# Performance work log

Measured on AMD Instinct MI355X. Metric: run time of the kernel, lower is better.

Reference implementation:

```python
import jax, jax.numpy as jnp
import numpy as np

B, T, DIM, H, L = 16, 4096, 256, 128, 3  # hidden = dim // 2, 3 bidirectional layers


def setup_inputs() -> dict:
    key = jax.random.key(0)
    kx, ki, kh, kb = jax.random.split(key, 4)
    x = jax.random.normal(kx, (B, T, DIM), dtype=jnp.float32)
    # stacked params: [layer, direction(0=fwd,1=bwd), ...]; gates packed as (r, z, n)
    Wi = jax.random.normal(ki, (L, 2, DIM, 3 * H), dtype=jnp.float32) / np.sqrt(DIM).astype(np.float32)
    Wh = jax.random.normal(kh, (L, 2, H, 3 * H), dtype=jnp.float32) / np.sqrt(H).astype(np.float32)
    bh = jax.random.normal(kb, (L, 2, 3 * H), dtype=jnp.float32) * 0.01
    return {"x": x, "Wi": Wi, "Wh": Wh, "bh": bh}


def _gru_dir(x, Wi, Wh, bh, reverse):
    """Run a GRU over time; x [B,T,D] -> h sequence [B,T,H].

    flax nnx.GRUCell math: input denses have no bias, hidden denses have bias;
    n-gate hidden contribution (incl. its bias) is gated by r.
    """
    # precompute all input-side gate projections in one big GEMM (efficient)
    xg = jnp.einsum('btd,dk->btk', x, Wi)  # [B,T,3H]
    Whr, Whz, Whn = jnp.split(Wh, 3, axis=1)
    bhr, bhz, bhn = jnp.split(bh, 3)

    def step(h, xg_t):
        xr, xz, xn = jnp.split(xg_t, 3, axis=-1)
        r = jax.nn.sigmoid(xr + h @ Whr + bhr)
        z = jax.nn.sigmoid(xz + h @ Whz + bhz)
        n = jnp.tanh(xn + r * (h @ Whn + bhn))
        h_new = (1.0 - z) * n + z * h
        return h_new, h_new

    h0 = jnp.zeros((x.shape[0], Whr.shape[0]), x.dtype)
    _, ys = jax.lax.scan(step, h0, jnp.swapaxes(xg, 0, 1), reverse=reverse)
    return jnp.swapaxes(ys, 0, 1)  # [B,T,H], time-aligned with input (keep_order)


def reference(x, Wi, Wh, bh):
    n_layers = Wi.shape[0]
    for l in range(n_layers):
        fwd = _gru_dir(x, Wi[l, 0], Wh[l, 0], bh[l, 0], reverse=False)
        bwd = _gru_dir(x, Wi[l, 1], Wh[l, 1], bh[l, 1], reverse=True)
        x = jnp.concatenate([fwd, bwd], axis=-1)  # [B,T,2H]=[B,T,DIM]
    return x
```

## Files before the change

### kernel.cpp

```cpp
#include <hip/hip_runtime.h>

#define BB 16
#define TT 4096
#define DD 256
#define HH 128
#define G3 384
#define MM (BB*TT)

typedef unsigned short u16;
typedef unsigned int u32;
typedef __attribute__((ext_vector_type(8))) short short8;
typedef __attribute__((ext_vector_type(4))) float f32x4;
typedef __attribute__((ext_vector_type(2))) unsigned int u32x2;

__device__ __forceinline__ float bf2f(u16 u) {
    return __uint_as_float(((u32)u) << 16);
}
__device__ __forceinline__ u16 f2bf(float f) {
    u32 u = __float_as_uint(f);
    u32 lsb = (u >> 16) & 1u;
    u += 0x7fffu + lsb;
    return (u16)(u >> 16);
}

#define Bb 128
#define Bn 128
#define Bk 16

__global__ __launch_bounds__(256) void gemm_in(const float* __restrict__ X,
                                               const float* __restrict__ Wi,
                                               float* __restrict__ XG) {
    __shared__ __align__(16) float As[Bk][Bb + 4];
    __shared__ __align__(16) float Bs[Bk][Bn + 4];
    const int tid = threadIdx.x;
    const int m0  = blockIdx.y * Bb;
    const int nb  = blockIdx.x;
    const int n0  = nb * Bn;
    const int dir = (n0 >= G3) ? 1 : 0;
    const int nloc0 = n0 - dir * G3;
    const float* Wd = Wi + (size_t)dir * DD * G3;

    const int tx = tid & 15;
    const int ty = tid >> 4;
    float acc[8][8];
    #pragma unroll
    for (int i = 0; i < 8; ++i)
        #pragma unroll
        for (int j = 0; j < 8; ++j) acc[i][j] = 0.f;

    for (int k0 = 0; k0 < DD; k0 += Bk) {
        #pragma unroll
        for (int p = 0; p < 2; ++p) {
            int idx = tid + p * 256;
            int row = idx >> 2;
            int c4  = (idx & 3) * 4;
            float4 v = *(const float4*)(X + (size_t)(m0 + row) * DD + k0 + c4);
            As[c4 + 0][row] = v.x;
            As[c4 + 1][row] = v.y;
            As[c4 + 2][row] = v.z;
            As[c4 + 3][row] = v.w;
        }
        #pragma unroll
        for (int p = 0; p < 2; ++p) {
            int idx  = tid + p * 256;
            int krow = idx >> 5;
            int c4   = (idx & 31) * 4;
            float4 v = *(const float4*)(Wd + (size_t)(k0 + krow) * G3 + nloc0 + c4);
            *(float4*)(&Bs[krow][c4]) = v;
        }
        __syncthreads();
        #pragma unroll
        for (int k = 0; k < Bk; ++k) {
            float4 a0 = *(const float4*)(&As[k][ty * 8]);
            float4 a1 = *(const float4*)(&As[k][ty * 8 + 4]);
            float4 b0 = *(const float4*)(&Bs[k][tx * 8]);
            float4 b1 = *(const float4*)(&Bs[k][tx * 8 + 4]);
            float av[8] = {a0.x, a0.y, a0.z, a0.w, a1.x, a1.y, a1.z, a1.w};
            float bv[8] = {b0.x, b0.y, b0.z, b0.w, b1.x, b1.y, b1.z, b1.w};
            #pragma unroll
            for (int i = 0; i < 8; ++i)
                #pragma unroll
                for (int j = 0; j < 8; ++j) acc[i][j] += av[i] * bv[j];
        }
        __syncthreads();
    }
    #pragma unroll
    for (int i = 0; i < 8; ++i) {
        int m = m0 + ty * 8 + i;
        float* dst = XG + ((size_t)dir * MM + m) * G3 + nloc0 + tx * 8;
        *(float4*)dst       = make_float4(acc[i][0], acc[i][1], acc[i][2], acc[i][3]);
        *(float4*)(dst + 4) = make_float4(acc[i][4], acc[i][5], acc[i][6], acc[i][7]);
    }
}

__device__ __forceinline__ float fast_sigmoid(float x) {
    float e = __expf(-x);
    return __builtin_amdgcn_rcpf(1.f + e);
}
__device__ __forceinline__ float fast_tanh(float x) {
    float e = __expf(2.f * x);
    return 1.f - 2.f * __builtin_amdgcn_rcpf(1.f + e);
}

__device__ __forceinline__ float permswap_add(float g) {
    u32 gu = __float_as_uint(g);
    u32x2 r = __builtin_amdgcn_permlane32_swap(gu, gu, false, false);
    return __uint_as_float(r[0]) + __uint_as_float(r[1]);
}

__device__ __forceinline__ u32 cvt_bf16(float f) {
    u32 pk;
    asm("v_cvt_pk_bf16_f32 %0, %1, %2" : "=v"(pk) : "v"(f), "v"(f));
    return pk;
}

struct XG3 { float r, z, n; };
__device__ __forceinline__ XG3 load3(const float* p) {
    XG3 v;
    v.r = p[0];
    v.z = p[128];
    v.n = p[256];
    return v;
}

#define HLO_OFF (2 * HH + 32)

__global__ __launch_bounds__(512, 1) void gru_rec(const float* __restrict__ XG,
                                                  const float* __restrict__ Wh,
                                                  const float* __restrict__ bh,
                                                  float* __restrict__ Xout) {
    const int wg   = blockIdx.x;
    const int dir  = wg & 1;
    const int b    = wg >> 1;
    const int tid  = threadIdx.x;
    const int lane = tid & 63;
    const int wave = tid >> 6;
    const int q    = lane >> 4;
    const int c    = lane & 15;
    const int hcol = wave * 16 + c;

    __shared__ __align__(16) u16 hbuf[HLO_OFF + 2 * HH];

    short8 bfr[3][4];
    {
        const float* W = Wh + (size_t)dir * HH * G3;
        #pragma unroll
        for (int g = 0; g < 3; ++g) {
            const int n = g * 128 + hcol;
            #pragma unroll
            for (int ch = 0; ch < 4; ++ch) {
                short8 vh;
                #pragma unroll
                for (int j = 0; j < 8; ++j) {
                    int k = ch * 32 + q * 8 + j;
                    vh[j] = (short)f2bf(W[(size_t)k * G3 + n]);
                }
                bfr[g][ch] = vh;
            }
        }
    }
    float hb[3];
    #pragma unroll
    for (int g = 0; g < 3; ++g) hb[g] = 0.5f * bh[dir * G3 + g * 128 + hcol];

    short8 a[4];
    #pragma unroll
    for (int ch = 0; ch < 4; ++ch)
        #pragma unroll
        for (int j = 0; j < 8; ++j) a[ch][j] = 0;
    float ho = 0.f;

    f32x4 accR = {0.f, 0.f, 0.f, 0.f};
    f32x4 accZ = {0.f, 0.f, 0.f, 0.f};
    f32x4 accN = {0.f, 0.f, 0.f, 0.f};

    const int t0    = dir ? (TT - 1) : 0;
    const int gstep = dir ? -G3 : G3;
    const int ostep = dir ? -DD : DD;

    const float* xp = XG + ((size_t)dir * MM + (size_t)b * TT + t0) * G3 + hcol;
    float* op = Xout + ((size_t)b * TT + t0) * DD + dir * HH + hcol;

    const u16* hrd = hbuf + ((c < 8) ? 0 : HLO_OFF) + q * 8;
    u16* hw_hi = hbuf + hcol;
    u16* hw_lo = hbuf + HLO_OFF + hcol;

    XG3 x0 = load3(xp);
    XG3 x1 = load3(xp + gstep);
    XG3 x2 = load3(xp + 2 * gstep);
    XG3 x3 = load3(xp + 3 * gstep);
    const float* xpf = xp + 4 * gstep;

#define SUBSTEP(S, XV, PK)                                                     \
    {                                                                          \
            \
        float xr = XV.r, xz = XV.z, xn = XV.n;                                 \
        if (t + (S) + 4 < TT) { XV = load3(xpf + (PK) * gstep); }              \
                  \
        accR[0] = __builtin_fmaf(0.5f, xr, hb[0]);                             \
        accZ[0] = __builtin_fmaf(0.5f, xz, hb[1]);                             \
        accN[0] = hb[2];                                                       \
                                   \
        _Pragma("unroll")                                                      \
        for (int ch = 0; ch < 4; ++ch) {                                       \
            accR = __builtin_amdgcn_mfma_f32_16x16x32_bf16(a[ch], bfr[0][ch], accR, 0, 0, 0); \
            accZ = __builtin_amdgcn_mfma_f32_16x16x32_bf16(a[ch], bfr[1][ch], accZ, 0, 0, 0); \
            accN = __builtin_amdgcn_mfma_f32_16x16x32_bf16(a[ch], bfr[2][ch], accN, 0, 0, 0); \
        }                                                                      \
        float pr = permswap_add(accR[0]);                                      \
        float pz = permswap_add(accZ[0]);                                      \
        float pm = permswap_add(accN[0]);                                      \
        float rg = fast_sigmoid(pr);                                           \
        float zg = fast_sigmoid(pz);                                           \
        float ng = fast_tanh(xn + rg * pm);                                    \
        float hn = (1.f - zg) * ng + zg * ho;                                  \
        ho = hn;                                                               \
                                 \
        u32 pk_hi = cvt_bf16(hn);                                              \
        float lo_f = hn - __uint_as_float(pk_hi << 16);                        \
        u32 pk_lo = cvt_bf16(lo_f);                                            \
        const int pb = ((S) + 1) & 1;                                          \
        if (q == 0) {                                                          \
            op[(S) * ostep] = hn;                                              \
            hw_hi[pb * HH]  = (u16)pk_hi;                                      \
        } else if (q == 1) {                                                   \
            hw_lo[pb * HH]  = (u16)pk_lo;                                      \
        }                                                                      \
        asm volatile("s_waitcnt lgkmcnt(0)\n\ts_barrier" ::: "memory");        \
        if (t + (S) + 1 < TT) {                                                \
            a[0] = *(const short8*)(hrd + pb * HH + 0);                        \
            a[1] = *(const short8*)(hrd + pb * HH + 32);                       \
            a[2] = *(const short8*)(hrd + pb * HH + 64);                       \
            a[3] = *(const short8*)(hrd + pb * HH + 96);                       \
        }                                                                      \
    }

    for (int t = 0; t < TT; t += 4) {
        SUBSTEP(0, x0, 0)
        SUBSTEP(1, x1, 1)
        xpf += 2 * gstep;
        SUBSTEP(2, x2, 0)
        SUBSTEP(3, x3, 1)
        xpf += 2 * gstep;
        op += 4 * ostep;
    }
#undef SUBSTEP
}

extern "C" void kernel_launch(void* const* d_in, const int* in_sizes, int n_in,
                              void* d_out, int out_size, void* d_ws, size_t ws_size,
                              hipStream_t stream) {
    const float* x  = (const float*)d_in[0];
    const float* Wi = (const float*)d_in[1];
    const float* Wh = (const float*)d_in[2];
    const float* bh = (const float*)d_in[3];
    float* out = (float*)d_out;

    float* XG = (float*)d_ws;

    for (int l = 0; l < 3; ++l) {
        const float* in  = (l == 0) ? x : out;
        const float* Wil = Wi + (size_t)l * 2 * DD * G3;
        const float* Whl = Wh + (size_t)l * 2 * HH * G3;
        const float* bhl = bh + (size_t)l * 2 * G3;

        gemm_in<<<dim3(6, MM / Bb), 256, 0, stream>>>(in, Wil, XG);
        gru_rec<<<32, 512, 0, stream>>>(XG, Whl, bhl, out);
    }
}
```

Measured before the change: 6.245 ms.

## Use split-bf16 MFMA (3-pass) for input projection GEMM

Replaces the FP32 FMA tiled GEMM for the input gate projections with an MFMA kernel. It splits each FP32 operand into bf16 hi and lo parts and accumulates hi*hi, hi*lo and lo*hi products to keep near-FP32 accuracy. The goal is to cut the cost of the large per-layer projection GEMM. The trade-offs are extra conversion work, strided weight loads and scalar output stores, and a small accuracy loss from dropping the lo*lo term.

Measured after the change: 5.667 ms. -9.2%, faster.

```diff
diff --git a/kernel.cpp b/kernel.cpp
--- a/kernel.cpp
+++ b/kernel.cpp
@@ -12,6 +12,7 @@
 typedef __attribute__((ext_vector_type(8))) short short8;
 typedef __attribute__((ext_vector_type(4))) float f32x4;
 typedef __attribute__((ext_vector_type(2))) unsigned int u32x2;
+typedef __attribute__((ext_vector_type(4))) unsigned int u32x4;
 
 __device__ __forceinline__ float bf2f(u16 u) {
     return __uint_as_float(((u32)u) << 16);
@@ -23,73 +24,117 @@
     return (u16)(u >> 16);
 }
 
-#define Bb 128
-#define Bn 128
-#define Bk 16
-
-__global__ __launch_bounds__(256) void gemm_in(const float* __restrict__ X,
-                                               const float* __restrict__ Wi,
-                                               float* __restrict__ XG) {
-    __shared__ __align__(16) float As[Bk][Bb + 4];
-    __shared__ __align__(16) float Bs[Bk][Bn + 4];
+__device__ __forceinline__ u32 cvt_pk2(float x, float y) {
+    u32 pk;
+    asm("v_cvt_pk_bf16_f32 %0, %1, %2" : "=v"(pk) : "v"(x), "v"(y));
+    return pk;
+}
+__device__ __forceinline__ u32 cvt_bf16(float f) {
+    u32 pk;
+    asm("v_cvt_pk_bf16_f32 %0, %1, %2" : "=v"(pk) : "v"(f), "v"(f));
+    return pk;
+}
+__device__ __forceinline__ void cvt2_hilo(float x, float y, u32& hi, u32& lo) {
+    u32 h = cvt_pk2(x, y);
+    float rx = x - __uint_as_float(h << 16);
+    float ry = y - __uint_as_float(h & 0xffff0000u);
+    hi = h;
+    lo = cvt_pk2(rx, ry);
+}
+
+#define GBM 128
+#define GBN 128
+#define GBK 32
+#define APAD 40
+
+__global__ __launch_bounds__(256, 2) void gemm_in(const float* __restrict__ X,
+                                                  const float* __restrict__ Wi,
+                                                  float* __restrict__ XG) {
+    __shared__ __align__(16) u16 Ahi[GBM][APAD];
+    __shared__ __align__(16) u16 Alo[GBM][APAD];
+    __shared__ __align__(16) u16 Bhi[GBN][APAD];
+    __shared__ __align__(16) u16 Blo[GBN][APAD];
+
     const int tid = threadIdx.x;
-    const int m0  = blockIdx.y * Bb;
-    const int nb  = blockIdx.x;
-    const int n0  = nb * Bn;
-    const int dir = (n0 >= G3) ? 1 : 0;
-    const int nloc0 = n0 - dir * G3;
+    const int m0  = blockIdx.y * GBM;
+    const int gc0 = blockIdx.x * GBN;
+    const int dir = (gc0 >= G3) ? 1 : 0;
+    const int n0  = gc0 - dir * G3;
     const float* Wd = Wi + (size_t)dir * DD * G3;
 
-    const int tx = tid & 15;
-    const int ty = tid >> 4;
-    float acc[8][8];
+    const int lane = tid & 63;
+    const int wv   = tid >> 6;
+    const int wr   = wv >> 1;
+    const int wc   = wv & 1;
+    const int q    = lane >> 4;
+    const int c    = lane & 15;
+
+    f32x4 acc[4][4];
     #pragma unroll
-    for (int i = 0; i < 8; ++i)
-        #pragma unroll
-        for (int j = 0; j < 8; ++j) acc[i][j] = 0.f;
-
-    for (int k0 = 0; k0 < DD; k0 += Bk) {
-        #pragma unroll
-        for (int p = 0; p < 2; ++p) {
+    for (int i = 0; i < 4; ++i)
+        #pragma unroll
+        for (int j = 0; j < 4; ++j) acc[i][j] = (f32x4){0.f, 0.f, 0.f, 0.f};
+
+    const int bn  = tid & 127;
+    const int bkh = (tid >> 7) * 16;
+
+    for (int k0 = 0; k0 < DD; k0 += GBK) {
+        #pragma unroll
+        for (int p = 0; p < 4; ++p) {
             int idx = tid + p * 256;
-            int row = idx >> 2;
-            int c4  = (idx & 3) * 4;
-            float4 v = *(const float4*)(X + (size_t)(m0 + row) * DD + k0 + c4);
-            As[c4 + 0][row] = v.x;
-            As[c4 + 1][row] = v.y;
-            As[c4 + 2][row] = v.z;
-            As[c4 + 3][row] = v.w;
-        }
-        #pragma unroll
-        for (int p = 0; p < 2; ++p) {
-            int idx  = tid + p * 256;
-            int krow = idx >> 5;
-            int c4   = (idx & 31) * 4;
-            float4 v = *(const float4*)(Wd + (size_t)(k0 + krow) * G3 + nloc0 + c4);
-            *(float4*)(&Bs[krow][c4]) = v;
+            int row = idx >> 3;
+            int k4  = (idx & 7) * 4;
+            float4 v = *(const float4*)(X + (size_t)(m0 + row) * DD + k0 + k4);
+            u32 h01, l01, h23, l23;
+            cvt2_hilo(v.x, v.y, h01, l01);
+            cvt2_hilo(v.z, v.w, h23, l23);
+            *(u32x2*)(&Ahi[row][k4]) = (u32x2){h01, h23};
+            *(u32x2*)(&Alo[row][k4]) = (u32x2){l01, l23};
+        }
+        {
+            float bv[16];
+            #pragma unroll
+            for (int j = 0; j < 16; ++j)
+                bv[j] = Wd[(size_t)(k0 + bkh + j) * G3 + n0 + bn];
+            u32 h[8], l[8];
+            #pragma unroll
+            for (int j = 0; j < 8; ++j)
+                cvt2_hilo(bv[2 * j], bv[2 * j + 1], h[j], l[j]);
+            *(u32x4*)(&Bhi[bn][bkh + 0]) = (u32x4){h[0], h[1], h[2], h[3]};
+            *(u32x4*)(&Bhi[bn][bkh + 8]) = (u32x4){h[4], h[5], h[6], h[7]};
+            *(u32x4*)(&Blo[bn][bkh + 0]) = (u32x4){l[0], l[1], l[2], l[3]};
+            *(u32x4*)(&Blo[bn][bkh + 8]) = (u32x4){l[4], l[5], l[6], l[7]};
         }
         __syncthreads();
-        #pragma unroll
-        for (int k = 0; k < Bk; ++k) {
-            float4 a0 = *(const float4*)(&As[k][ty * 8]);
-            float4 a1 = *(const float4*)(&As[k][ty * 8 + 4]);
-            float4 b0 = *(const float4*)(&Bs[k][tx * 8]);
-            float4 b1 = *(const float4*)(&Bs[k][tx * 8 + 4]);
-            float av[8] = {a0.x, a0.y, a0.z, a0.w, a1.x, a1.y, a1.z, a1.w};
-            float bv[8] = {b0.x, b0.y, b0.z, b0.w, b1.x, b1.y, b1.z, b1.w};
-            #pragma unroll
-            for (int i = 0; i < 8; ++i)
-                #pragma unroll
-                for (int j = 0; j < 8; ++j) acc[i][j] += av[i] * bv[j];
-        }
+        short8 afh[4], afl[4], bfh[4], bfl[4];
+        #pragma unroll
+        for (int i = 0; i < 4; ++i) {
+            afh[i] = *(const short8*)(&Ahi[wr * 64 + i * 16 + c][q * 8]);
+            afl[i] = *(const short8*)(&Alo[wr * 64 + i * 16 + c][q * 8]);
+            bfh[i] = *(const short8*)(&Bhi[wc * 64 + i * 16 + c][q * 8]);
+            bfl[i] = *(const short8*)(&Blo[wc * 64 + i * 16 + c][q * 8]);
+        }
+        #pragma unroll
+        for (int i = 0; i < 4; ++i)
+            #pragma unroll
+            for (int j = 0; j < 4; ++j) {
+                acc[i][j] = __builtin_amdgcn_mfma_f32_16x16x32_bf16(afh[i], bfh[j], acc[i][j], 0, 0, 0);
+                acc[i][j] = __builtin_amdgcn_mfma_f32_16x16x32_bf16(afh[i], bfl[j], acc[i][j], 0, 0, 0);
+                acc[i][j] = __builtin_amdgcn_mfma_f32_16x16x32_bf16(afl[i], bfh[j], acc[i][j], 0, 0, 0);
+            }
         __syncthreads();
     }
     #pragma unroll
-    for (int i = 0; i < 8; ++i) {
-        int m = m0 + ty * 8 + i;
-        float* dst = XG + ((size_t)dir * MM + m) * G3 + nloc0 + tx * 8;
-        *(float4*)dst       = make_float4(acc[i][0], acc[i][1], acc[i][2], acc[i][3]);
-        *(float4*)(dst + 4) = make_float4(acc[i][4], acc[i][5], acc[i][6], acc[i][7]);
+    for (int i = 0; i < 4; ++i) {
+        #pragma unroll
+        for (int j = 0; j < 4; ++j) {
+            const int n = n0 + wc * 64 + j * 16 + c;
+            #pragma unroll
+            for (int r = 0; r < 4; ++r) {
+                const int m = m0 + wr * 64 + i * 16 + q * 4 + r;
+                XG[((size_t)dir * MM + m) * G3 + n] = acc[i][j][r];
+            }
+        }
     }
 }
 
@@ -106,12 +151,6 @@
     u32 gu = __float_as_uint(g);
     u32x2 r = __builtin_amdgcn_permlane32_swap(gu, gu, false, false);
     return __uint_as_float(r[0]) + __uint_as_float(r[1]);
-}
-
-__device__ __forceinline__ u32 cvt_bf16(float f) {
-    u32 pk;
-    asm("v_cvt_pk_bf16_f32 %0, %1, %2" : "=v"(pk) : "v"(f), "v"(f));
-    return pk;
 }
 
 struct XG3 { float r, z, n; };
@@ -264,7 +303,7 @@
         const float* Whl = Wh + (size_t)l * 2 * HH * G3;
         const float* bhl = bh + (size_t)l * 2 * G3;
 
-        gemm_in<<<dim3(6, MM / Bb), 256, 0, stream>>>(in, Wil, XG);
+        gemm_in<<<dim3(6, MM / GBM), 256, 0, stream>>>(in, Wil, XG);
         gru_rec<<<32, 512, 0, stream>>>(XG, Whl, bhl, out);
     }
 }
```
